# Kernel tuning notes

Hardware: AMD Instinct MI355X
Metric: run time of the kernel (lower is better)

The kernel has to match this reference:

```python
import jax, jax.numpy as jnp
import numpy as np

# Transformer-XL relative multi-head attention (eval mode, dropout = identity)
B, Q, M, D, H = 2, 1024, 1024, 1024, 16
DH = D // H          # 64 head dim
K = Q + M            # key length = memory + current segment
SCALE = 0.02         # param init scale


def setup_inputs() -> dict:
    key = jax.random.key(0)
    ks = jax.random.split(key, 10)
    return {
        "inputs": jax.random.normal(ks[0], (B, Q, D), jnp.float32),
        "inputs_mem": jax.random.normal(ks[1], (B, M, D), jnp.float32),
        "r": jax.random.normal(ks[2], (B, K, D), jnp.float32),
        "W_qkv": jax.random.normal(ks[3], (D, 3 * D), jnp.float32) * SCALE,
        "b_qkv": jnp.zeros((3 * D,), jnp.float32),
        "W_r": jax.random.normal(ks[4], (D, D), jnp.float32) * SCALE,
        "b_r": jnp.zeros((D,), jnp.float32),
        "W_o": jax.random.normal(ks[5], (D, D), jnp.float32) * SCALE,
        "b_o": jnp.zeros((D,), jnp.float32),
        "u": jax.random.normal(ks[6], (1, H, 1, DH), jnp.float32) * SCALE,
        "v": jax.random.normal(ks[7], (1, H, 1, DH), jnp.float32) * SCALE,
    }


def _split_heads(x):
    # [B, L, D] -> [B, H, L, DH]
    b, l, _ = x.shape
    return x.reshape(b, l, H, DH).transpose(0, 2, 1, 3)


def _rel_shift(x):
    # Transformer-XL relative shift: pad one zero column on the left,
    # reshape to [B, H, K+1, Q], drop first row, reshape back.
    b, h, q, k = x.shape
    x = jnp.pad(x, ((0, 0), (0, 0), (0, 0), (1, 0)))
    x = x.reshape(b, h, k + 1, q)[:, :, 1:, :]
    return x.reshape(b, h, q, k)


def reference(inputs, inputs_mem, r, W_qkv, b_qkv, W_r, b_r, W_o, b_o, u, v):
    cat = jnp.concatenate([inputs_mem, inputs], axis=1)      # [B, K, D]
    w = cat @ W_qkv + b_qkv                                   # [B, K, 3D]
    rp = r @ W_r + b_r                                        # [B, K, D]
    # NOTE: source splits as (q, v, k) in that order
    w_q, w_v, w_k = jnp.split(w, 3, axis=-1)
    hq = _split_heads(w_q)[:, :, -Q:]                          # [B, H, Q, DH]
    hk = _split_heads(w_k)                                     # [B, H, K, DH]
    hv = _split_heads(w_v)                                     # [B, H, K, DH]
    hr = _split_heads(rp)                                      # [B, H, K, DH]
    ac = jnp.einsum('bhqd,bhkd->bhqk', hq + u, hk)             # content term
    bd = _rel_shift(jnp.einsum('bhqd,bhkd->bhqk', hq + v, hr)) # position term
    score = (ac + bd) / (DH ** 0.5)
    # causal mask with memory: query i attends to all mem + positions <= i
    mem_len = K - Q
    mask = (jnp.arange(K)[None, :] <= mem_len + jnp.arange(Q)[:, None]).astype(jnp.float32)
    score = score * mask - 1e30 * (1.0 - mask)
    weights = jax.nn.softmax(score, axis=-1)                   # [B, H, Q, K]
    out = jnp.einsum('bhqk,bhkd->bhqd', weights, hv)           # [B, H, Q, DH]
    out = out.transpose(0, 2, 1, 3).reshape(B, Q, D)
    return out @ W_o + b_o
```

## Files before the change

kernel.cpp:

```cpp
#include <hip/hip_runtime.h>
#include <hip/hip_bf16.h>
#include <stdint.h>


typedef __bf16 bf16;
typedef __bf16 bf16x2 __attribute__((ext_vector_type(2)));
typedef __bf16 bf16x4 __attribute__((ext_vector_type(4)));
typedef __bf16 bf16x8 __attribute__((ext_vector_type(8)));
typedef float  f32x4  __attribute__((ext_vector_type(4)));

__device__ __forceinline__ void async_copy16(void* lds, const void* g) {
    auto gp = (const __attribute__((address_space(1))) void*)(uintptr_t)g;
    auto lp = (__attribute__((address_space(3))) void*)(uint32_t)(uintptr_t)lds;
    __builtin_amdgcn_global_load_lds(gp, lp, 16, 0, 0);
}

__device__ __forceinline__ void gemm128_core(
    const bf16* __restrict__ A, const bf16* __restrict__ Bt, const int Kd,
    const int m0, const int n0, bf16* As, bf16* Bs, f32x4 acc[4][4])
{
    const int tid  = threadIdx.x;
    const int lane = tid & 63;
    const int wave = tid >> 6;
    const int wr   = (wave >> 1) * 64;
    const int wc   = (wave & 1) * 64;
    const int lr   = lane & 15;
    const int q4   = lane >> 4;

#pragma unroll
    for (int i = 0; i < 4; ++i)
#pragma unroll
        for (int j = 0; j < 4; ++j) {
            acc[i][j][0] = 0.f; acc[i][j][1] = 0.f; acc[i][j][2] = 0.f; acc[i][j][3] = 0.f;
        }

    for (int k0 = 0; k0 < Kd; k0 += 32) {
#pragma unroll
        for (int it = 0; it < 2; ++it) {
            const int cb0   = (it * 4 + wave) * 64;
            const int chunk = cb0 + lane;
            const int row   = chunk >> 2;
            const int cg    = (chunk & 3) * 8;
            async_copy16(As + cb0 * 8, A  + (size_t)(m0 + row) * Kd + k0 + cg);
            async_copy16(Bs + cb0 * 8, Bt + (size_t)(n0 + row) * Kd + k0 + cg);
        }
        __syncthreads();
        bf16x8 af[4], bfr[4];
#pragma unroll
        for (int rb = 0; rb < 4; ++rb)
            af[rb] = *(const bf16x8*)&As[(wr + rb * 16 + lr) * 32 + q4 * 8];
#pragma unroll
        for (int cb = 0; cb < 4; ++cb)
            bfr[cb] = *(const bf16x8*)&Bs[(wc + cb * 16 + lr) * 32 + q4 * 8];
#pragma unroll
        for (int rb = 0; rb < 4; ++rb)
#pragma unroll
            for (int cb = 0; cb < 4; ++cb)
                acc[rb][cb] = __builtin_amdgcn_mfma_f32_16x16x32_bf16(af[rb], bfr[cb], acc[rb][cb], 0, 0, 0);
        __syncthreads();
    }
}

__global__ __launch_bounds__(256) void k_prep_w(
    const float* __restrict__ Wqkv, const float* __restrict__ Wr,
    const float* __restrict__ Wo,
    bf16* __restrict__ Wqkvt, bf16* __restrict__ Wrt, bf16* __restrict__ Wot)
{
    __shared__ float t[32][33];
    int id = blockIdx.x;
    const float* in; bf16* out; int C, bx, by;
    if (id < 3072)      { in = Wqkv; out = Wqkvt; C = 3072; bx = id % 96; by = id / 96; }
    else if (id < 4096) { id -= 3072; in = Wr; out = Wrt; C = 1024; bx = id & 31; by = id >> 5; }
    else                { id -= 4096; in = Wo; out = Wot; C = 1024; bx = id & 31; by = id >> 5; }
    const int R = 1024;
    const int c0 = bx * 32, r0 = by * 32;
    const int lc = threadIdx.x & 31, lrow = threadIdx.x >> 5;
#pragma unroll
    for (int p = 0; p < 4; ++p)
        t[lrow + p * 8][lc] = in[(size_t)(r0 + lrow + p * 8) * C + c0 + lc];
    __syncthreads();
#pragma unroll
    for (int p = 0; p < 4; ++p)
        out[(size_t)(c0 + lrow + p * 8) * R + r0 + lc] = (bf16)t[lc][lrow + p * 8];
}

__global__ __launch_bounds__(256) void k_prep_x(
    const float* __restrict__ mem, const float* __restrict__ inp,
    const float* __restrict__ r,
    bf16* __restrict__ catb, bf16* __restrict__ rb)
{
    const int id = blockIdx.x;
    if (id < 4096) {
        const int e   = (id * 256 + threadIdx.x) * 4;
        const int row = e >> 10, dc = e & 1023;
        const int b   = row >> 11, k = row & 2047;
        const float* src = (k < 1024) ? mem + ((size_t)b * 1024 + k) * 1024 + dc
                                      : inp + ((size_t)b * 1024 + (k - 1024)) * 1024 + dc;
        float4 f = *(const float4*)src;
        bf16x4 o; o[0] = (bf16)f.x; o[1] = (bf16)f.y; o[2] = (bf16)f.z; o[3] = (bf16)f.w;
        *(bf16x4*)&catb[e] = o;
    } else {
        const int e = ((id - 4096) * 256 + threadIdx.x) * 4;
        float4 f = *(const float4*)(r + e);
        bf16x4 o; o[0] = (bf16)f.x; o[1] = (bf16)f.y; o[2] = (bf16)f.z; o[3] = (bf16)f.w;
        *(bf16x4*)&rb[e] = o;
    }
}

__global__ __launch_bounds__(256) void k_gemm_qkvr(
    const bf16* __restrict__ catb, const bf16* __restrict__ Wqkvt,
    const float* __restrict__ b_qkv, const float* __restrict__ u, const float* __restrict__ v,
    const bf16* __restrict__ rb_, const bf16* __restrict__ Wrt,
    const float* __restrict__ b_r,
    bf16* __restrict__ hq_u, bf16* __restrict__ hq_v,
    bf16* __restrict__ hk, bf16* __restrict__ hvT, bf16* __restrict__ hr)
{
    __shared__ bf16 lds[2 * 128 * 32];
    f32x4 acc[4][4];
    const int m0 = blockIdx.x * 128;
    const int lane = threadIdx.x & 63, wave = threadIdx.x >> 6;
    const int wr = (wave >> 1) * 64, wc = (wave & 1) * 64;
    const int lr = lane & 15, q4 = lane >> 4;

    if (blockIdx.y < 24) {
        const int n0 = blockIdx.y * 128;
        gemm128_core(catb, Wqkvt, 1024, m0, n0, lds, lds + 128 * 32, acc);
#pragma unroll
        for (int rb = 0; rb < 4; ++rb) {
#pragma unroll
            for (int cb = 0; cb < 4; ++cb) {
                const int col  = n0 + wc + cb * 16 + lr;
                const int part = col >> 10;
                const int hd   = col & 1023;
                const int h    = hd >> 6, d = hd & 63;
                const float bcol = b_qkv[col];
#pragma unroll
                for (int r = 0; r < 4; ++r) {
                    const int row = m0 + wr + rb * 16 + q4 * 4 + r;
                    const int b   = row >> 11, k = row & 2047;
                    const float val = acc[rb][cb][r] + bcol;
                    if (part == 0) {
                        if (k >= 1024) {
                            const size_t o = (((size_t)(b * 16 + h)) * 1024 + (k - 1024)) * 64 + d;
                            hq_u[o] = (bf16)(val + u[hd]);
                            hq_v[o] = (bf16)(val + v[hd]);
                        }
                    } else if (part == 1) {
                        hvT[(((size_t)(b * 16 + h)) * 64 + d) * 2048 + k] = (bf16)val;
                    } else {
                        hk[(((size_t)(b * 16 + h)) * 2048 + k) * 64 + d] = (bf16)val;
                    }
                }
            }
        }
    } else {
        const int n0 = (blockIdx.y - 24) * 128;
        gemm128_core(rb_, Wrt, 1024, m0, n0, lds, lds + 128 * 32, acc);
#pragma unroll
        for (int rb = 0; rb < 4; ++rb) {
#pragma unroll
            for (int cb = 0; cb < 4; ++cb) {
                const int col = n0 + wc + cb * 16 + lr;
                const int h = col >> 6, d = col & 63;
                const float bcol = b_r[col];
#pragma unroll
                for (int r = 0; r < 4; ++r) {
                    const int row = m0 + wr + rb * 16 + q4 * 4 + r;
                    const int b = row >> 11, k = row & 2047;
                    hr[(((size_t)(b * 16 + h)) * 2048 + k) * 64 + d] = (bf16)(acc[rb][cb][r] + bcol);
                }
            }
        }
    }
}

__global__ __launch_bounds__(256) void k_gemm_out(
    const bf16* __restrict__ attn, const bf16* __restrict__ Wt,
    const float* __restrict__ bias, float* __restrict__ out)
{
    __shared__ bf16 lds[2 * 128 * 32];
    f32x4 acc[4][4];
    const int m0 = blockIdx.x * 128, n0 = blockIdx.y * 128;
    gemm128_core(attn, Wt, 1024, m0, n0, lds, lds + 128 * 32, acc);

    const int lane = threadIdx.x & 63, wave = threadIdx.x >> 6;
    const int wr = (wave >> 1) * 64, wc = (wave & 1) * 64;
    const int lr = lane & 15, q4 = lane >> 4;
#pragma unroll
    for (int rb = 0; rb < 4; ++rb) {
#pragma unroll
        for (int cb = 0; cb < 4; ++cb) {
            const int col = n0 + wc + cb * 16 + lr;
            const float bcol = bias[col];
#pragma unroll
            for (int r = 0; r < 4; ++r) {
                const int row = m0 + wr + rb * 16 + q4 * 4 + r;
                out[(size_t)row * 1024 + col] = acc[rb][cb][r] + bcol;
            }
        }
    }
}

__global__ __launch_bounds__(256) void k_attn(
    const bf16* __restrict__ hq_u, const bf16* __restrict__ hq_v,
    const bf16* __restrict__ hk, const bf16* __restrict__ hvT,
    const bf16* __restrict__ hr, bf16* __restrict__ attn)
{
    __shared__ bf16 Ks[2][64][72];
    __shared__ bf16 Vt[2][64][72];
    __shared__ bf16 Rs[192 * 72];
    __shared__ bf16 U[4][1600];

    const int bh = blockIdx.y;
    const int qt = (bh & 16) ? (15 - (int)blockIdx.x) : (int)blockIdx.x;
    const int q0 = qt * 64;
    const int tid = threadIdx.x, lane = tid & 63, wave = tid >> 6;
    const int lr = lane & 15, q4 = lane >> 4;
    bf16* Uw = &U[wave][0];

    const int nt  = 17 + qt;
    const int m0c = 15 - qt;
    const size_t kvbase = (size_t)bh * 2048 * 64;

    const int ci0  = tid,        r0_ = ci0 >> 3,  c0_ = (ci0 & 7) * 8;
    const int ci1  = 256 + tid,  r1_ = ci1 >> 3,  c1_ = (ci1 & 7) * 8;

    bf16x8 kv0, kv1, vv0, vv1, rv0, rv1;
    auto load_kv = [&](int t) {
        const int k0 = t * 64;
        kv0 = *(const bf16x8*)&hk [kvbase + (size_t)(k0 + r0_) * 64 + c0_];
        kv1 = *(const bf16x8*)&hk [kvbase + (size_t)(k0 + r1_) * 64 + c1_];
        vv0 = *(const bf16x8*)&hvT[kvbase + (size_t)r0_ * 2048 + k0 + c0_];
        vv1 = *(const bf16x8*)&hvT[kvbase + (size_t)r1_ * 2048 + k0 + c1_];
    };
    auto load_r = [&](int c) {
        if (c * 64 < 2048) {
            rv0 = *(const bf16x8*)&hr[kvbase + (size_t)(c * 64 + r0_) * 64 + c0_];
            rv1 = *(const bf16x8*)&hr[kvbase + (size_t)(c * 64 + r1_) * 64 + c1_];
        } else {
#pragma unroll
            for (int z = 0; z < 8; ++z) { rv0[z] = (bf16)0.f; rv1[z] = (bf16)0.f; }
        }
    };
    auto write_kv = [&](int buf) {
        *(bf16x8*)&Ks[buf][r0_][c0_] = kv0;
        *(bf16x8*)&Ks[buf][r1_][c1_] = kv1;
        *(bf16x8*)&Vt[buf][r0_][c0_] = vv0;
        *(bf16x8*)&Vt[buf][r1_][c1_] = vv1;
    };
    auto write_r = [&](int slot) {
        *(bf16x8*)&Rs[(slot * 64 + r0_) * 72 + c0_] = rv0;
        *(bf16x8*)&Rs[(slot * 64 + r1_) * 72 + c1_] = rv1;
    };

    const size_t qrow = ((size_t)bh * 1024 + q0 + wave * 16 + lr) * 64;
    const bf16x8 qu0 = *(const bf16x8*)&hq_u[qrow + q4 * 8];
    const bf16x8 qu1 = *(const bf16x8*)&hq_u[qrow + 32 + q4 * 8];
    const bf16x8 qv0 = *(const bf16x8*)&hq_v[qrow + q4 * 8];
    const bf16x8 qv1 = *(const bf16x8*)&hq_v[qrow + 32 + q4 * 8];

    f32x4 Oacc[4];
#pragma unroll
    for (int i = 0; i < 4; ++i) { Oacc[i][0] = 0.f; Oacc[i][1] = 0.f; Oacc[i][2] = 0.f; Oacc[i][3] = 0.f; }
    float lp[4] = {0.f, 0.f, 0.f, 0.f};

    load_kv(0);  write_kv(0);
    load_r(m0c);     write_r(m0c % 3);
    load_r(m0c + 1); write_r((m0c + 1) % 3);
    __syncthreads();

    for (int t = 0; t < nt; ++t) {
        const int k0  = t * 64;
        const int mt  = m0c + t;
        const int s0  = mt % 3;
        const int s1  = (s0 + 1 == 3) ? 0 : s0 + 1;
        const int s2  = (s1 + 1 == 3) ? 0 : s1 + 1;
        const int buf = t & 1;
        const bool more = (t + 1 < nt);
        if (more) { load_kv(t + 1); load_r(mt + 2); }

        __builtin_amdgcn_s_setprio(1);
        f32x4 S[4];
#pragma unroll
        for (int cb = 0; cb < 4; ++cb) {
            const bf16x8 kf0 = *(const bf16x8*)&Ks[buf][cb * 16 + lr][q4 * 8];
            const bf16x8 kf1 = *(const bf16x8*)&Ks[buf][cb * 16 + lr][32 + q4 * 8];
            f32x4 z; z[0] = 0.f; z[1] = 0.f; z[2] = 0.f; z[3] = 0.f;
            z = __builtin_amdgcn_mfma_f32_16x16x32_bf16(qu0, kf0, z, 0, 0, 0);
            S[cb] = __builtin_amdgcn_mfma_f32_16x16x32_bf16(qu1, kf1, z, 0, 0, 0);
        }
#pragma unroll
        for (int jbi = 0; jbi < 5; ++jbi) {
            const int jb   = jbi + 3 - wave;
            const int rrow = ((jb & 4) ? s1 : s0) * 64 + (jb & 3) * 16 + lr;
            const bf16x8 rf0 = *(const bf16x8*)&Rs[rrow * 72 + q4 * 8];
            const bf16x8 rf1 = *(const bf16x8*)&Rs[rrow * 72 + 32 + q4 * 8];
            f32x4 z; z[0] = 0.f; z[1] = 0.f; z[2] = 0.f; z[3] = 0.f;
            z = __builtin_amdgcn_mfma_f32_16x16x32_bf16(qv0, rf0, z, 0, 0, 0);
            z = __builtin_amdgcn_mfma_f32_16x16x32_bf16(qv1, rf1, z, 0, 0, 0);
            bf16x4 pk;
            pk[0] = (bf16)z[0]; pk[1] = (bf16)z[1]; pk[2] = (bf16)z[2]; pk[3] = (bf16)z[3];
            *(bf16x4*)&Uw[(jbi * 16 + lr) * 20 + q4 * 4] = pk;
        }

        float bdv[4][4];
#pragma unroll
        for (int cb = 0; cb < 4; ++cb)
#pragma unroll
            for (int r = 0; r < 4; ++r) {
                const int tq = q4 * 4 + r;
                bdv[cb][r] = (float)Uw[(cb * 16 + lr + 15 - tq) * 20 + tq];
            }

#pragma unroll
        for (int cb = 0; cb < 4; ++cb) {
            const int k = k0 + cb * 16 + lr;
#pragma unroll
            for (int r = 0; r < 4; ++r) {
                const int q = q0 + wave * 16 + q4 * 4 + r;
                const float s = (S[cb][r] + bdv[cb][r]) * 0.125f;
                const float p = (k <= 1024 + q) ? __expf(s) : 0.f;
                lp[r] += p;
                Uw[(q4 * 4 + r) * 76 + cb * 16 + lr] = (bf16)p;
            }
        }

        const bf16x8 pf0 = *(const bf16x8*)&Uw[lr * 76 + q4 * 8];
        const bf16x8 pf1 = *(const bf16x8*)&Uw[lr * 76 + 32 + q4 * 8];
#pragma unroll
        for (int db = 0; db < 4; ++db) {
            const bf16x8 vf0 = *(const bf16x8*)&Vt[buf][db * 16 + lr][q4 * 8];
            const bf16x8 vf1 = *(const bf16x8*)&Vt[buf][db * 16 + lr][32 + q4 * 8];
            Oacc[db] = __builtin_amdgcn_mfma_f32_16x16x32_bf16(pf0, vf0, Oacc[db], 0, 0, 0);
            Oacc[db] = __builtin_amdgcn_mfma_f32_16x16x32_bf16(pf1, vf1, Oacc[db], 0, 0, 0);
        }
        __builtin_amdgcn_s_setprio(0);

        if (more) {
            write_kv(buf ^ 1);
            write_r(s2);
            __syncthreads();
        }
    }

#pragma unroll
    for (int off = 1; off < 16; off <<= 1)
#pragma unroll
        for (int r = 0; r < 4; ++r) lp[r] += __shfl_xor(lp[r], off, 64);

    const int b = bh >> 4, h = bh & 15;
#pragma unroll
    for (int r = 0; r < 4; ++r) {
        const float rl = 1.f / lp[r];
        const int q = q0 + wave * 16 + q4 * 4 + r;
#pragma unroll
        for (int db = 0; db < 4; ++db) {
            const int d = db * 16 + lr;
            attn[(((size_t)b * 1024 + q) * 16 + h) * 64 + d] = (bf16)(Oacc[db][r] * rl);
        }
    }
}

extern "C" void kernel_launch(void* const* d_in, const int* in_sizes, int n_in,
                              void* d_out, int out_size, void* d_ws, size_t ws_size,
                              hipStream_t stream)
{
    const float* inputs = (const float*)d_in[0];
    const float* mem    = (const float*)d_in[1];
    const float* r      = (const float*)d_in[2];
    const float* W_qkv  = (const float*)d_in[3];
    const float* b_qkv  = (const float*)d_in[4];
    const float* W_r    = (const float*)d_in[5];
    const float* b_r    = (const float*)d_in[6];
    const float* W_o    = (const float*)d_in[7];
    const float* b_o    = (const float*)d_in[8];
    const float* u      = (const float*)d_in[9];
    const float* v      = (const float*)d_in[10];
    float* out = (float*)d_out;

    char* ws = (char*)d_ws;
    size_t off = 0;
    auto alloc = [&](size_t bytes) -> void* {
        void* p = ws + off;
        off += (bytes + 255) & ~(size_t)255;
        return p;
    };
    bf16* hq_u  = (bf16*)alloc(2ull * 16 * 1024 * 64 * 2);
    bf16* hq_v  = (bf16*)alloc(2ull * 16 * 1024 * 64 * 2);
    bf16* hk    = (bf16*)alloc(2ull * 16 * 2048 * 64 * 2);
    bf16* hvT   = (bf16*)alloc(2ull * 16 * 2048 * 64 * 2);
    bf16* hr    = (bf16*)alloc(2ull * 16 * 2048 * 64 * 2);
    bf16* attnb = (bf16*)alloc(2ull * 1024 * 1024 * 2);
    bf16* Wot   = (bf16*)alloc(1024ull * 1024 * 2);
    bf16* catb  = (bf16*)alloc(4096ull * 1024 * 2);
    bf16* rb    = (bf16*)alloc(4096ull * 1024 * 2);
    bf16* Wqkvt = (bf16*)alloc(3072ull * 1024 * 2);
    bf16* Wrt   = (bf16*)alloc(1024ull * 1024 * 2);

    k_prep_w<<<5120, 256, 0, stream>>>(W_qkv, W_r, W_o, Wqkvt, Wrt, Wot);
    k_prep_x<<<8192, 256, 0, stream>>>(mem, inputs, r, catb, rb);

    k_gemm_qkvr<<<dim3(32, 32), 256, 0, stream>>>(catb, Wqkvt, b_qkv, u, v,
                                                  rb, Wrt, b_r,
                                                  hq_u, hq_v, hk, hvT, hr);
    k_attn<<<dim3(16, 32), 256, 0, stream>>>(hq_u, hq_v, hk, hvT, hr, attnb);
    k_gemm_out<<<dim3(16, 8), 256, 0, stream>>>(attnb, Wot, b_o, out);
}
```

Measured before the change: 261.7 us.

## Skip Q projection for memory rows and use 64-row tiles for output GEMM

The QKV GEMM previously computed the Q projection for all 2048 key rows and then discarded the memory half. Now Q tiles are computed only for the current-segment rows, which cuts the grid from 32x32 to 32x28 blocks. The output projection moves from 128x128 to 64x128 tiles, doubling its block count to 256 so more CUs are busy on this small GEMM. The trade-off is lower per-block data reuse in the output GEMM.

After: 249.9 us. -4.5%, faster.

```diff
diff --git a/kernel.cpp b/kernel.cpp
--- a/kernel.cpp
+++ b/kernel.cpp
@@ -54,6 +54,57 @@
             bfr[cb] = *(const bf16x8*)&Bs[(wc + cb * 16 + lr) * 32 + q4 * 8];
 #pragma unroll
         for (int rb = 0; rb < 4; ++rb)
+#pragma unroll
+            for (int cb = 0; cb < 4; ++cb)
+                acc[rb][cb] = __builtin_amdgcn_mfma_f32_16x16x32_bf16(af[rb], bfr[cb], acc[rb][cb], 0, 0, 0);
+        __syncthreads();
+    }
+}
+
+__device__ __forceinline__ void gemm64_core(
+    const bf16* __restrict__ A, const bf16* __restrict__ Bt, const int Kd,
+    const int m0, const int n0, bf16* As, bf16* Bs, f32x4 acc[2][4])
+{
+    const int tid  = threadIdx.x;
+    const int lane = tid & 63;
+    const int wave = tid >> 6;
+    const int wr   = (wave >> 1) * 32;
+    const int wc   = (wave & 1) * 64;
+    const int lr   = lane & 15;
+    const int q4   = lane >> 4;
+
+#pragma unroll
+    for (int i = 0; i < 2; ++i)
+#pragma unroll
+        for (int j = 0; j < 4; ++j) {
+            acc[i][j][0] = 0.f; acc[i][j][1] = 0.f; acc[i][j][2] = 0.f; acc[i][j][3] = 0.f;
+        }
+
+    for (int k0 = 0; k0 < Kd; k0 += 32) {
+        {
+            const int chunk = tid;
+            const int row   = chunk >> 2;
+            const int cg    = (chunk & 3) * 8;
+            async_copy16(As + (wave * 64) * 8, A + (size_t)(m0 + row) * Kd + k0 + cg);
+        }
+#pragma unroll
+        for (int it = 0; it < 2; ++it) {
+            const int cb0   = (it * 4 + wave) * 64;
+            const int chunk = cb0 + lane;
+            const int row   = chunk >> 2;
+            const int cg    = (chunk & 3) * 8;
+            async_copy16(Bs + cb0 * 8, Bt + (size_t)(n0 + row) * Kd + k0 + cg);
+        }
+        __syncthreads();
+        bf16x8 af[2], bfr[4];
+#pragma unroll
+        for (int rb = 0; rb < 2; ++rb)
+            af[rb] = *(const bf16x8*)&As[(wr + rb * 16 + lr) * 32 + q4 * 8];
+#pragma unroll
+        for (int cb = 0; cb < 4; ++cb)
+            bfr[cb] = *(const bf16x8*)&Bs[(wc + cb * 16 + lr) * 32 + q4 * 8];
+#pragma unroll
+        for (int rb = 0; rb < 2; ++rb)
 #pragma unroll
             for (int cb = 0; cb < 4; ++cb)
                 acc[rb][cb] = __builtin_amdgcn_mfma_f32_16x16x32_bf16(af[rb], bfr[cb], acc[rb][cb], 0, 0, 0);
@@ -117,13 +168,14 @@
 {
     __shared__ bf16 lds[2 * 128 * 32];
     f32x4 acc[4][4];
-    const int m0 = blockIdx.x * 128;
     const int lane = threadIdx.x & 63, wave = threadIdx.x >> 6;
     const int wr = (wave >> 1) * 64, wc = (wave & 1) * 64;
     const int lr = lane & 15, q4 = lane >> 4;
-
-    if (blockIdx.y < 24) {
-        const int n0 = blockIdx.y * 128;
+    const int y = blockIdx.y;
+
+    if (y < 16) {
+        const int m0 = blockIdx.x * 128;
+        const int n0 = 1024 + y * 128;
         gemm128_core(catb, Wqkvt, 1024, m0, n0, lds, lds + 128 * 32, acc);
 #pragma unroll
         for (int rb = 0; rb < 4; ++rb) {
@@ -139,13 +191,7 @@
                     const int row = m0 + wr + rb * 16 + q4 * 4 + r;
                     const int b   = row >> 11, k = row & 2047;
                     const float val = acc[rb][cb][r] + bcol;
-                    if (part == 0) {
-                        if (k >= 1024) {
-                            const size_t o = (((size_t)(b * 16 + h)) * 1024 + (k - 1024)) * 64 + d;
-                            hq_u[o] = (bf16)(val + u[hd]);
-                            hq_v[o] = (bf16)(val + v[hd]);
-                        }
-                    } else if (part == 1) {
+                    if (part == 1) {
                         hvT[(((size_t)(b * 16 + h)) * 64 + d) * 2048 + k] = (bf16)val;
                     } else {
                         hk[(((size_t)(b * 16 + h)) * 2048 + k) * 64 + d] = (bf16)val;
@@ -153,8 +199,34 @@
                 }
             }
         }
+    } else if (y < 20) {
+        const int linear = (y - 16) * 32 + blockIdx.x;
+        const int n0 = (linear & 7) * 128;
+        const int mi = linear >> 3;
+        const int m0 = (mi >> 3) * 2048 + 1024 + (mi & 7) * 128;
+        gemm128_core(catb, Wqkvt, 1024, m0, n0, lds, lds + 128 * 32, acc);
+#pragma unroll
+        for (int rb = 0; rb < 4; ++rb) {
+#pragma unroll
+            for (int cb = 0; cb < 4; ++cb) {
+                const int col = n0 + wc + cb * 16 + lr;
+                const int h = col >> 6, d = col & 63;
+                const float bcol = b_qkv[col];
+                const float uc = u[col], vc = v[col];
+#pragma unroll
+                for (int r = 0; r < 4; ++r) {
+                    const int row = m0 + wr + rb * 16 + q4 * 4 + r;
+                    const int b   = row >> 11, k = row & 2047;
+                    const float val = acc[rb][cb][r] + bcol;
+                    const size_t o = (((size_t)(b * 16 + h)) * 1024 + (k - 1024)) * 64 + d;
+                    hq_u[o] = (bf16)(val + uc);
+                    hq_v[o] = (bf16)(val + vc);
+                }
+            }
+        }
     } else {
-        const int n0 = (blockIdx.y - 24) * 128;
+        const int m0 = blockIdx.x * 128;
+        const int n0 = (y - 20) * 128;
         gemm128_core(rb_, Wrt, 1024, m0, n0, lds, lds + 128 * 32, acc);
 #pragma unroll
         for (int rb = 0; rb < 4; ++rb) {
@@ -178,16 +250,16 @@
     const bf16* __restrict__ attn, const bf16* __restrict__ Wt,
     const float* __restrict__ bias, float* __restrict__ out)
 {
-    __shared__ bf16 lds[2 * 128 * 32];
-    f32x4 acc[4][4];
-    const int m0 = blockIdx.x * 128, n0 = blockIdx.y * 128;
-    gemm128_core(attn, Wt, 1024, m0, n0, lds, lds + 128 * 32, acc);
+    __shared__ bf16 lds[64 * 32 + 128 * 32];
+    f32x4 acc[2][4];
+    const int m0 = blockIdx.x * 64, n0 = blockIdx.y * 128;
+    gemm64_core(attn, Wt, 1024, m0, n0, lds, lds + 64 * 32, acc);
 
     const int lane = threadIdx.x & 63, wave = threadIdx.x >> 6;
-    const int wr = (wave >> 1) * 64, wc = (wave & 1) * 64;
+    const int wr = (wave >> 1) * 32, wc = (wave & 1) * 64;
     const int lr = lane & 15, q4 = lane >> 4;
 #pragma unroll
-    for (int rb = 0; rb < 4; ++rb) {
+    for (int rb = 0; rb < 2; ++rb) {
 #pragma unroll
         for (int cb = 0; cb < 4; ++cb) {
             const int col = n0 + wc + cb * 16 + lr;
@@ -400,9 +472,9 @@
     k_prep_w<<<5120, 256, 0, stream>>>(W_qkv, W_r, W_o, Wqkvt, Wrt, Wot);
     k_prep_x<<<8192, 256, 0, stream>>>(mem, inputs, r, catb, rb);
 
-    k_gemm_qkvr<<<dim3(32, 32), 256, 0, stream>>>(catb, Wqkvt, b_qkv, u, v,
+    k_gemm_qkvr<<<dim3(32, 28), 256, 0, stream>>>(catb, Wqkvt, b_qkv, u, v,
                                                   rb, Wrt, b_r,
                                                   hq_u, hq_v, hk, hvT, hr);
     k_attn<<<dim3(16, 32), 256, 0, stream>>>(hq_u, hq_v, hk, hvT, hr, attnb);
-    k_gemm_out<<<dim3(16, 8), 256, 0, stream>>>(attnb, Wot, b_o, out);
-}
+    k_gemm_out<<<dim3(32, 8), 256, 0, stream>>>(attnb, Wot, b_o, out);
+}
```
